# Performance work log

Hardware: AMD Instinct MI355X
Metric: run time of the kernel (lower is better)

## Reference

```python
import jax, jax.numpy as jnp
import numpy as np

N = 100000
E = 1600000
D_IN = 128
D_OUT = 128
EPS_GIN = 0.0  # GIN epsilon from __init__
LN_EPS = 1e-5
PROJ_EPS = 1e-9


def setup_inputs() -> dict:
    key = jax.random.key(0)
    ks = jax.random.split(key, 9)
    x = jax.random.normal(ks[0], (N, D_IN), dtype=jnp.float32)
    edge_index = jax.random.randint(ks[1], (2, E), 0, N, dtype=jnp.int64)
    edge_weight = jax.random.normal(ks[2], (E,), dtype=jnp.float32)
    # MLP params (Linear(in,out) -> ReLU -> Linear(out,out)), torch default-ish init
    s1 = 1.0 / np.sqrt(D_IN)
    s2 = 1.0 / np.sqrt(D_OUT)
    W1 = jax.random.uniform(ks[3], (D_IN, D_OUT), jnp.float32, -s1, s1)
    b1 = jax.random.uniform(ks[4], (D_OUT,), jnp.float32, -s1, s1)
    W2 = jax.random.uniform(ks[5], (D_OUT, D_OUT), jnp.float32, -s2, s2)
    b2 = jax.random.uniform(ks[6], (D_OUT,), jnp.float32, -s2, s2)
    gamma = jnp.ones((D_OUT,), jnp.float32)
    beta = jnp.zeros((D_OUT,), jnp.float32)
    return {"x": x, "edge_index": edge_index, "edge_weight": edge_weight,
            "W1": W1, "b1": b1, "W2": W2, "b2": b2, "gamma": gamma, "beta": beta}


def _aggregate(x, edge_index, edge_weight):
    # Per-target-node softmax over edge weights, then weighted projective average.
    src = edge_index[0]
    tgt = edge_index[1]
    n = x.shape[0]
    m = jax.ops.segment_max(edge_weight, tgt, num_segments=n)          # [N]
    ew = jnp.exp(edge_weight - m[tgt])                                  # [E], stable softmax numerator
    denom = jax.ops.segment_sum(ew, tgt, num_segments=n)               # [N]
    w = ew / denom[tgt]                                                 # [E], per-node softmax weights
    msg = w[:, None] * x[src]                                           # [E, D]
    agg = jax.ops.segment_sum(msg, tgt, num_segments=n)                # [N, D] weighted sum
    # projective_average: normalize the weighted combination to the unit sphere
    norm = jnp.linalg.norm(agg, axis=-1, keepdims=True)
    return agg / (norm + PROJ_EPS)                                      # zero rows stay zero


def _layer_norm(h, gamma, beta):
    mu = jnp.mean(h, axis=-1, keepdims=True)
    var = jnp.var(h, axis=-1, keepdims=True)
    return gamma * (h - mu) * jax.lax.rsqrt(var + LN_EPS) + beta


def reference(x, edge_index, edge_weight, W1, b1, W2, b2, gamma, beta):
    neigh = _aggregate(x, edge_index, edge_weight)
    combined = (1.0 + EPS_GIN) * x + neigh
    h = jnp.maximum(combined @ W1 + b1, 0.0)
    h = h @ W2 + b2
    h = _layer_norm(h, gamma, beta)
    # dropout: eval mode -> identity
    return h
```

## Files before the change

kernel.cpp:

```cpp
#include <hip/hip_runtime.h>
#include <hip/hip_bf16.h>

#define D 128
#define CH 2048
#define BSH 9
#define SLAB 9216
#define PREP_BLK 1024

typedef __attribute__((ext_vector_type(8))) short short8;
typedef __attribute__((ext_vector_type(4))) float f32x4;
typedef __attribute__((ext_vector_type(4))) int int4v;
typedef __attribute__((ext_vector_type(2))) int int2v;
typedef __attribute__((ext_vector_type(4))) float float4v;
typedef __attribute__((ext_vector_type(2))) float float2v;
typedef __attribute__((ext_vector_type(4))) unsigned uint4v;
typedef __attribute__((ext_vector_type(2))) unsigned uint2v;
typedef _Float16 half2_t __attribute__((ext_vector_type(2)));

__device__ __forceinline__ unsigned short us_bf16(float f) {
    return __bfloat16_as_ushort(__float2bfloat16(f));
}
__device__ __forceinline__ unsigned pack_bf16(float a, float b) {
    return (unsigned)us_bf16(a) | ((unsigned)us_bf16(b) << 16);
}
__device__ __forceinline__ unsigned pack_f16(float a, float b) {
    unsigned short ua = __builtin_bit_cast(unsigned short, (_Float16)a);
    unsigned short ub = __builtin_bit_cast(unsigned short, (_Float16)b);
    return (unsigned)ua | ((unsigned)ub << 16);
}
__device__ __forceinline__ float f16_lo(int y) {
    return (float)__builtin_bit_cast(_Float16, (unsigned short)(y & 0xffff));
}
__device__ __forceinline__ half2_t as_h2(unsigned u) {
    return __builtin_bit_cast(half2_t, u);
}
__device__ __forceinline__ int2v nt_load2(const int2* p) {
    return __builtin_nontemporal_load(reinterpret_cast<const int2v*>(p));
}

__global__ __launch_bounds__(256) void k_prepbinA(
    const int* __restrict__ src, const int* __restrict__ tgt,
    const float* __restrict__ ew, int* __restrict__ bcnt,
    int2* __restrict__ stage, int E, int nbuk, int nchunk,
    const float* __restrict__ x, unsigned* __restrict__ xh,
    unsigned* __restrict__ xq, int nf4,
    const float* __restrict__ W1, const float* __restrict__ W2,
    unsigned short* __restrict__ W1t, unsigned short* __restrict__ W2t)
{
    __shared__ int2 recs[CH];
    __shared__ unsigned short bslot[CH];
    __shared__ int sh[256];
    __shared__ int lbase[256];
    __shared__ int gofs[256];

    int tid = threadIdx.x;

    if (blockIdx.x >= (unsigned)nchunk) {
        int pb = blockIdx.x - nchunk;
        int i0 = pb * 256 + tid;
        int stride = PREP_BLK * 256;
        const float4v* x4 = reinterpret_cast<const float4v*>(x);
        uint2v* xh2 = reinterpret_cast<uint2v*>(xh);
        for (int i = i0; i < nf4; i += stride) {
            float4v v = x4[i];
            uint2v o;
            o.x = pack_f16(v.x, v.y);
            o.y = pack_f16(v.z, v.w);
            xh2[i] = o;
            int p = __builtin_amdgcn_cvt_pk_fp8_f32(v.x, v.y, 0, false);
            p = __builtin_amdgcn_cvt_pk_fp8_f32(v.z, v.w, p, true);
            xq[i] = (unsigned)p;
        }
        if (i0 < 16384) {
            int k = i0 >> 7, nn = i0 & 127;
            W1t[nn * 128 + k] = us_bf16(W1[i0]);
            W2t[nn * 128 + k] = us_bf16(W2[i0]);
        }
        return;
    }

    int c0 = blockIdx.x * CH;
    int chunkCnt = min(CH, E - c0);

    sh[tid] = 0;
    __syncthreads();

    int myb[8], mypos[8], mysrc[8]; unsigned myy[8];
    #pragma unroll
    for (int k = 0; k < 8; ++k) {
        int idx = k * 256 + tid;
        myb[k] = -1;
        if (idx < chunkCnt) {
            int e = c0 + idx;
            int t = __builtin_nontemporal_load(&tgt[e]);
            int b = t >> BSH;
            float expw = __expf(__builtin_nontemporal_load(&ew[e]));
            unsigned short h = __builtin_bit_cast(unsigned short, (_Float16)expw);
            myb[k] = b;
            myy[k] = ((unsigned)(t & ((1 << BSH) - 1)) << 16) | (unsigned)h;
            mysrc[k] = __builtin_nontemporal_load(&src[e]);
            mypos[k] = atomicAdd(&sh[b], 1);
        }
    }
    __syncthreads();
    int cnt_b = sh[tid];
    for (int off = 1; off < 256; off <<= 1) {
        int o = (tid >= off) ? sh[tid - off] : 0;
        __syncthreads();
        sh[tid] += o;
        __syncthreads();
    }
    int lb = sh[tid] - cnt_b;
    lbase[tid] = lb;
    if (cnt_b > 0 && tid < nbuk) {
        int gb = atomicAdd(&bcnt[tid], cnt_b) + tid * SLAB;
        gofs[tid] = gb - lb;
    }
    __syncthreads();
    #pragma unroll
    for (int k = 0; k < 8; ++k) {
        if (myb[k] >= 0) {
            int slot = lbase[myb[k]] + mypos[k];
            recs[slot] = make_int2(mysrc[k], (int)myy[k]);
            bslot[slot] = (unsigned short)myb[k];
        }
    }
    __syncthreads();
    for (int i = tid; i < chunkCnt; i += 256) {
        int b = bslot[i];
        stage[gofs[b] + i] = recs[i];
    }
}

__global__ __launch_bounds__(256) void k_binB(
    const int* __restrict__ bcnt, const int2* __restrict__ stage,
    int2* __restrict__ csr, int* __restrict__ rowptr, int n)
{
    __shared__ int lcnt[1 << BSH];
    __shared__ int sc[256];
    int b = blockIdx.x;
    int tid = threadIdx.x;
    int node0 = b << BSH;
    int nn = min(1 << BSH, n - node0);
    int s0 = b * SLAB;
    int s1 = s0 + bcnt[b];

    for (int j = tid; j < (1 << BSH); j += 256) lcnt[j] = 0;
    __syncthreads();

    for (int i = s0 + tid; i < s1; i += 256) {
        int2v rec = nt_load2(&stage[i]);
        atomicAdd(&lcnt[((unsigned)rec.y) >> 16], 1);
    }
    __syncthreads();

    int v0 = lcnt[2 * tid], v1 = lcnt[2 * tid + 1];
    int tsum = v0 + v1;
    sc[tid] = tsum;
    __syncthreads();
    for (int off = 1; off < 256; off <<= 1) {
        int o = (tid >= off) ? sc[tid - off] : 0;
        __syncthreads();
        sc[tid] += o;
        __syncthreads();
    }
    int excl = sc[tid] - tsum;
    int p0 = s0 + excl, p1 = s0 + excl + v0;
    if (2 * tid < nn)     rowptr[node0 + 2 * tid] = p0;
    if (2 * tid + 1 < nn) rowptr[node0 + 2 * tid + 1] = p1;
    __syncthreads();
    lcnt[2 * tid] = p0;
    lcnt[2 * tid + 1] = p1;
    __syncthreads();

    for (int i = s0 + tid; i < s1; i += 256) {
        int2v rec = nt_load2(&stage[i]);
        int pos = atomicAdd(&lcnt[((unsigned)rec.y) >> 16], 1);
        csr[pos] = make_int2(rec.x, rec.y);
    }
}

__global__ __launch_bounds__(256) void k_agg(
    const int* __restrict__ rowptr, const int* __restrict__ bcnt,
    const int2* __restrict__ csr,
    const uint4v* __restrict__ xq4, const uint4v* __restrict__ xh4,
    uint4v* __restrict__ cmb4, int n)
{
    int w = threadIdx.x >> 6;
    int lane = threadIdx.x & 63;
    int node = blockIdx.x * 4 + w;
    if (node >= n) node = n - 1;

    int b = node >> BSH;
    int r0 = rowptr[node];
    int r1;
    if ((((node + 1) & ((1 << BSH) - 1)) == 0) || (node + 1 >= n))
        r1 = b * SLAB + bcnt[b];
    else
        r1 = rowptr[node + 1];
    int cnt = r1 - r0;

    int eg = lane >> 3;
    int dg = lane & 7;

    float a[16];
    #pragma unroll
    for (int j = 0; j < 16; ++j) a[j] = 0.f;

    int last = (cnt > 0) ? cnt - 1 : 0;
    for (int base = 0; base < cnt; base += 32) {
        #pragma unroll
        for (int i = 0; i < 4; ++i) {
            if (base + i * 8 >= cnt) break;
            int e = base + i * 8 + eg;
            bool valid = e < cnt;
            int2v cr = nt_load2(&csr[r0 + (valid ? e : last)]);
            float wn = valid ? f16_lo(cr.y) : 0.f;
            uint4v q = xq4[cr.x * 8 + dg];
            #pragma unroll
            for (int h = 0; h < 4; ++h) {
                int word = (int)((h == 0) ? q.x : (h == 1) ? q.y : (h == 2) ? q.z : q.w);
                float2v flo = __builtin_amdgcn_cvt_pk_f32_fp8(word, false);
                float2v fhi = __builtin_amdgcn_cvt_pk_f32_fp8(word, true);
                a[h * 4 + 0] = fmaf(wn, flo.x, a[h * 4 + 0]);
                a[h * 4 + 1] = fmaf(wn, flo.y, a[h * 4 + 1]);
                a[h * 4 + 2] = fmaf(wn, fhi.x, a[h * 4 + 2]);
                a[h * 4 + 3] = fmaf(wn, fhi.y, a[h * 4 + 3]);
            }
        }
    }

    #pragma unroll
    for (int j = 0; j < 16; ++j) a[j] *= 0.00390625f;
    unsigned u[8];
    #pragma unroll
    for (int j = 0; j < 8; ++j)
        u[j] = __builtin_bit_cast(unsigned,
                   __builtin_amdgcn_cvt_pkrtz(a[2 * j], a[2 * j + 1]));
    #pragma unroll
    for (int m = 8; m <= 32; m <<= 1)
        #pragma unroll
        for (int j = 0; j < 8; ++j) {
            half2_t s = as_h2(u[j]) + as_h2((unsigned)__shfl_xor((int)u[j], m));
            u[j] = __builtin_bit_cast(unsigned, s);
        }
    float af[16];
    #pragma unroll
    for (int j = 0; j < 8; ++j) {
        half2_t s = as_h2(u[j]);
        af[2 * j] = (float)s.x;
        af[2 * j + 1] = (float)s.y;
    }

    float ss = 0.f;
    #pragma unroll
    for (int j = 0; j < 16; ++j) ss = fmaf(af[j], af[j], ss);
    #pragma unroll
    for (int m = 1; m <= 4; m <<= 1) ss += __shfl_xor(ss, m);
    float rn = 1.f / (sqrtf(ss) + 1e-9f);

    if (eg == 0) {
        #pragma unroll
        for (int h = 0; h < 2; ++h) {
            uint4v hx = xh4[node * 16 + dg * 2 + h];
            half2_t x0 = as_h2(hx.x), x1 = as_h2(hx.y), x2 = as_h2(hx.z), x3 = as_h2(hx.w);
            const float* ah = &af[h * 8];
            uint4v o;
            o.x = pack_bf16((float)x0.x + ah[0] * rn, (float)x0.y + ah[1] * rn);
            o.y = pack_bf16((float)x1.x + ah[2] * rn, (float)x1.y + ah[3] * rn);
            o.z = pack_bf16((float)x2.x + ah[4] * rn, (float)x2.y + ah[5] * rn);
            o.w = pack_bf16((float)x3.x + ah[6] * rn, (float)x3.y + ah[7] * rn);
            cmb4[node * 16 + dg * 2 + h] = o;
        }
    }
}

__global__ __launch_bounds__(256) void k_mlp(
    const uint4v* __restrict__ cmb4,
    const unsigned short* __restrict__ W1t, const unsigned short* __restrict__ W2t,
    const float* __restrict__ b1, const float* __restrict__ b2,
    const float* __restrict__ gamma, const float* __restrict__ beta,
    float* __restrict__ out, int n)
{
    __shared__ __align__(16) unsigned short sA[64][136];

    int node0 = blockIdx.x * 64;
    int w = threadIdx.x >> 6;
    int lane = threadIdx.x & 63;
    int lr = lane & 15;
    int lg = lane >> 4;
    int mr = w * 16;

    for (int idx = threadIdx.x; idx < 64 * 16; idx += 256) {
        int row = idx >> 4, seg = idx & 15;
        int gr = node0 + row; if (gr >= n) gr = n - 1;
        uint4v v = cmb4[gr * 16 + seg];
        *reinterpret_cast<uint4v*>(&sA[row][seg * 8]) = v;
    }
    __syncthreads();

    short8 aF[4];
    #pragma unroll
    for (int kt = 0; kt < 4; ++kt)
        aF[kt] = *reinterpret_cast<const short8*>(&sA[mr + lr][kt * 32 + lg * 8]);

    #pragma unroll
    for (int nt = 0; nt < 8; ++nt) {
        f32x4 c = {0.f, 0.f, 0.f, 0.f};
        #pragma unroll
        for (int kt = 0; kt < 4; ++kt) {
            short8 bF = *reinterpret_cast<const short8*>(
                &W1t[(nt * 16 + lr) * 128 + kt * 32 + lg * 8]);
            c = __builtin_amdgcn_mfma_f32_16x16x32_bf16(aF[kt], bF, c, 0, 0, 0);
        }
        float b1v = b1[nt * 16 + lr];
        #pragma unroll
        for (int reg = 0; reg < 4; ++reg) {
            float h = fmaxf(c[reg] + b1v, 0.f);
            sA[mr + lg * 4 + reg][nt * 16 + lr] = us_bf16(h);
        }
    }
    __syncthreads();

    short8 a2F[4];
    #pragma unroll
    for (int kt = 0; kt < 4; ++kt)
        a2F[kt] = *reinterpret_cast<const short8*>(&sA[mr + lr][kt * 32 + lg * 8]);

    f32x4 c2[8];
    float b2v[8], gv[8], bev[8];
    #pragma unroll
    for (int nt = 0; nt < 8; ++nt) {
        c2[nt] = (f32x4){0.f, 0.f, 0.f, 0.f};
        #pragma unroll
        for (int kt = 0; kt < 4; ++kt) {
            short8 bF = *reinterpret_cast<const short8*>(
                &W2t[(nt * 16 + lr) * 128 + kt * 32 + lg * 8]);
            c2[nt] = __builtin_amdgcn_mfma_f32_16x16x32_bf16(a2F[kt], bF, c2[nt], 0, 0, 0);
        }
        int col = nt * 16 + lr;
        b2v[nt] = b2[col]; gv[nt] = gamma[col]; bev[nt] = beta[col];
    }

    float rs[4] = {0.f, 0.f, 0.f, 0.f}, sq[4] = {0.f, 0.f, 0.f, 0.f};
    #pragma unroll
    for (int nt = 0; nt < 8; ++nt)
        #pragma unroll
        for (int reg = 0; reg < 4; ++reg) {
            float v = c2[nt][reg] + b2v[nt];
            rs[reg] += v; sq[reg] += v * v;
        }
    #pragma unroll
    for (int off = 1; off <= 8; off <<= 1)
        #pragma unroll
        for (int reg = 0; reg < 4; ++reg) {
            rs[reg] += __shfl_xor(rs[reg], off);
            sq[reg] += __shfl_xor(sq[reg], off);
        }
    float mu[4], rstd[4];
    #pragma unroll
    for (int reg = 0; reg < 4; ++reg) {
        mu[reg] = rs[reg] * (1.f / 128.f);
        float var = sq[reg] * (1.f / 128.f) - mu[reg] * mu[reg];
        rstd[reg] = rsqrtf(var + 1e-5f);
    }

    #pragma unroll
    for (int nt = 0; nt < 8; ++nt)
        #pragma unroll
        for (int reg = 0; reg < 4; ++reg) {
            int gr = node0 + mr + lg * 4 + reg;
            if (gr < n) {
                float v = c2[nt][reg] + b2v[nt];
                out[gr * 128 + nt * 16 + lr] = gv[nt] * (v - mu[reg]) * rstd[reg] + bev[nt];
            }
        }
}

extern "C" void kernel_launch(void* const* d_in, const int* in_sizes, int n_in,
                              void* d_out, int out_size, void* d_ws, size_t ws_size,
                              hipStream_t stream) {
    const float* x     = (const float*)d_in[0];
    const int*   ei    = (const int*)d_in[1];
    const float* ew    = (const float*)d_in[2];
    const float* W1    = (const float*)d_in[3];
    const float* b1    = (const float*)d_in[4];
    const float* W2    = (const float*)d_in[5];
    const float* b2    = (const float*)d_in[6];
    const float* gamma = (const float*)d_in[7];
    const float* beta  = (const float*)d_in[8];

    int n = in_sizes[0] / D;
    int E = in_sizes[2];
    const int* src = ei;
    const int* tgt = ei + E;

    int nbuk = (n + (1 << BSH) - 1) >> BSH;

    char* ws = (char*)d_ws;
    int2*     csr    = (int2*)ws;     ws += (size_t)nbuk * SLAB * sizeof(int2);
    unsigned* xh     = (unsigned*)ws; ws += (size_t)n * 64 * sizeof(unsigned);
    unsigned* xq     = (unsigned*)ws; ws += (size_t)n * 32 * sizeof(unsigned);
    unsigned* cmb    = (unsigned*)ws; ws += (size_t)n * 64 * sizeof(unsigned);
    unsigned short* W1t = (unsigned short*)ws; ws += 128 * 128 * sizeof(unsigned short);
    unsigned short* W2t = (unsigned short*)ws; ws += 128 * 128 * sizeof(unsigned short);
    int*      rowptr = (int*)ws;      ws += ((size_t)n + 1) * sizeof(int);
    int*      bcnt   = (int*)ws;      ws += 256 * sizeof(int);
    int2*     stage  = (int2*)cmb;

    hipMemsetAsync((void*)bcnt, 0, 256 * sizeof(int), stream);

    int nf4 = n * D / 4;
    int nchunk = (E + CH - 1) / CH;
    k_prepbinA<<<nchunk + PREP_BLK, 256, 0, stream>>>(
        src, tgt, ew, bcnt, stage, E, nbuk, nchunk,
        x, xh, xq, nf4, W1, W2, W1t, W2t);

    k_binB<<<nbuk, 256, 0, stream>>>(bcnt, stage, csr, rowptr, n);

    k_agg<<<(n + 3) / 4, 256, 0, stream>>>(rowptr, bcnt, csr,
                                           (const uint4v*)xq, (const uint4v*)xh,
                                           (uint4v*)cmb, n);

    k_mlp<<<(n + 63) / 64, 256, 0, stream>>>((const uint4v*)cmb, W1t, W2t,
                                             b1, b2, gamma, beta,
                                             (float*)d_out, n);
}
```

Before: 202.0 us.

## Fuse neighbor aggregation and MLP into one kernel via shared memory

Merges the aggregation and MLP kernels so each 512-thread block aggregates 64 nodes (8 per wave) directly into a shared-memory tile, then four waves run the MFMA MLP on it. This removes the global round trip of the bf16 combined buffer and one kernel launch. The staging buffer gets its own workspace region. The cost is that half the waves sit idle during the MLP phase, and each wave now processes nodes serially, with fewer blocks available to hide gather latency.

```diff
diff --git a/kernel.cpp b/kernel.cpp
--- a/kernel.cpp
+++ b/kernel.cpp
@@ -180,103 +180,10 @@
     }
 }
 
-__global__ __launch_bounds__(256) void k_agg(
+__global__ __launch_bounds__(512) void k_aggmlp(
     const int* __restrict__ rowptr, const int* __restrict__ bcnt,
     const int2* __restrict__ csr,
     const uint4v* __restrict__ xq4, const uint4v* __restrict__ xh4,
-    uint4v* __restrict__ cmb4, int n)
-{
-    int w = threadIdx.x >> 6;
-    int lane = threadIdx.x & 63;
-    int node = blockIdx.x * 4 + w;
-    if (node >= n) node = n - 1;
-
-    int b = node >> BSH;
-    int r0 = rowptr[node];
-    int r1;
-    if ((((node + 1) & ((1 << BSH) - 1)) == 0) || (node + 1 >= n))
-        r1 = b * SLAB + bcnt[b];
-    else
-        r1 = rowptr[node + 1];
-    int cnt = r1 - r0;
-
-    int eg = lane >> 3;
-    int dg = lane & 7;
-
-    float a[16];
-    #pragma unroll
-    for (int j = 0; j < 16; ++j) a[j] = 0.f;
-
-    int last = (cnt > 0) ? cnt - 1 : 0;
-    for (int base = 0; base < cnt; base += 32) {
-        #pragma unroll
-        for (int i = 0; i < 4; ++i) {
-            if (base + i * 8 >= cnt) break;
-            int e = base + i * 8 + eg;
-            bool valid = e < cnt;
-            int2v cr = nt_load2(&csr[r0 + (valid ? e : last)]);
-            float wn = valid ? f16_lo(cr.y) : 0.f;
-            uint4v q = xq4[cr.x * 8 + dg];
-            #pragma unroll
-            for (int h = 0; h < 4; ++h) {
-                int word = (int)((h == 0) ? q.x : (h == 1) ? q.y : (h == 2) ? q.z : q.w);
-                float2v flo = __builtin_amdgcn_cvt_pk_f32_fp8(word, false);
-                float2v fhi = __builtin_amdgcn_cvt_pk_f32_fp8(word, true);
-                a[h * 4 + 0] = fmaf(wn, flo.x, a[h * 4 + 0]);
-                a[h * 4 + 1] = fmaf(wn, flo.y, a[h * 4 + 1]);
-                a[h * 4 + 2] = fmaf(wn, fhi.x, a[h * 4 + 2]);
-                a[h * 4 + 3] = fmaf(wn, fhi.y, a[h * 4 + 3]);
-            }
-        }
-    }
-
-    #pragma unroll
-    for (int j = 0; j < 16; ++j) a[j] *= 0.00390625f;
-    unsigned u[8];
-    #pragma unroll
-    for (int j = 0; j < 8; ++j)
-        u[j] = __builtin_bit_cast(unsigned,
-                   __builtin_amdgcn_cvt_pkrtz(a[2 * j], a[2 * j + 1]));
-    #pragma unroll
-    for (int m = 8; m <= 32; m <<= 1)
-        #pragma unroll
-        for (int j = 0; j < 8; ++j) {
-            half2_t s = as_h2(u[j]) + as_h2((unsigned)__shfl_xor((int)u[j], m));
-            u[j] = __builtin_bit_cast(unsigned, s);
-        }
-    float af[16];
-    #pragma unroll
-    for (int j = 0; j < 8; ++j) {
-        half2_t s = as_h2(u[j]);
-        af[2 * j] = (float)s.x;
-        af[2 * j + 1] = (float)s.y;
-    }
-
-    float ss = 0.f;
-    #pragma unroll
-    for (int j = 0; j < 16; ++j) ss = fmaf(af[j], af[j], ss);
-    #pragma unroll
-    for (int m = 1; m <= 4; m <<= 1) ss += __shfl_xor(ss, m);
-    float rn = 1.f / (sqrtf(ss) + 1e-9f);
-
-    if (eg == 0) {
-        #pragma unroll
-        for (int h = 0; h < 2; ++h) {
-            uint4v hx = xh4[node * 16 + dg * 2 + h];
-            half2_t x0 = as_h2(hx.x), x1 = as_h2(hx.y), x2 = as_h2(hx.z), x3 = as_h2(hx.w);
-            const float* ah = &af[h * 8];
-            uint4v o;
-            o.x = pack_bf16((float)x0.x + ah[0] * rn, (float)x0.y + ah[1] * rn);
-            o.y = pack_bf16((float)x1.x + ah[2] * rn, (float)x1.y + ah[3] * rn);
-            o.z = pack_bf16((float)x2.x + ah[4] * rn, (float)x2.y + ah[5] * rn);
-            o.w = pack_bf16((float)x3.x + ah[6] * rn, (float)x3.y + ah[7] * rn);
-            cmb4[node * 16 + dg * 2 + h] = o;
-        }
-    }
-}
-
-__global__ __launch_bounds__(256) void k_mlp(
-    const uint4v* __restrict__ cmb4,
     const unsigned short* __restrict__ W1t, const unsigned short* __restrict__ W2t,
     const float* __restrict__ b1, const float* __restrict__ b2,
     const float* __restrict__ gamma, const float* __restrict__ beta,
@@ -284,20 +191,105 @@
 {
     __shared__ __align__(16) unsigned short sA[64][136];
 
+    int tid = threadIdx.x;
+    int wv = tid >> 6;
+    int lane = tid & 63;
     int node0 = blockIdx.x * 64;
-    int w = threadIdx.x >> 6;
-    int lane = threadIdx.x & 63;
+
+    int eg = lane >> 3;
+    int dg = lane & 7;
+
+    for (int r = wv * 8; r < wv * 8 + 8; ++r) {
+        int node = node0 + r;
+        if (node >= n) node = n - 1;
+
+        int b = node >> BSH;
+        int r0 = rowptr[node];
+        int r1;
+        if ((((node + 1) & ((1 << BSH) - 1)) == 0) || (node + 1 >= n))
+            r1 = b * SLAB + bcnt[b];
+        else
+            r1 = rowptr[node + 1];
+        int cnt = r1 - r0;
+
+        float a[16];
+        #pragma unroll
+        for (int j = 0; j < 16; ++j) a[j] = 0.f;
+
+        int last = (cnt > 0) ? cnt - 1 : 0;
+        for (int base = 0; base < cnt; base += 32) {
+            #pragma unroll
+            for (int i = 0; i < 4; ++i) {
+                if (base + i * 8 >= cnt) break;
+                int e = base + i * 8 + eg;
+                bool valid = e < cnt;
+                int2v cr = nt_load2(&csr[r0 + (valid ? e : last)]);
+                float wn = valid ? f16_lo(cr.y) : 0.f;
+                uint4v q = xq4[cr.x * 8 + dg];
+                #pragma unroll
+                for (int h = 0; h < 4; ++h) {
+                    int word = (int)((h == 0) ? q.x : (h == 1) ? q.y : (h == 2) ? q.z : q.w);
+                    float2v flo = __builtin_amdgcn_cvt_pk_f32_fp8(word, false);
+                    float2v fhi = __builtin_amdgcn_cvt_pk_f32_fp8(word, true);
+                    a[h * 4 + 0] = fmaf(wn, flo.x, a[h * 4 + 0]);
+                    a[h * 4 + 1] = fmaf(wn, flo.y, a[h * 4 + 1]);
+                    a[h * 4 + 2] = fmaf(wn, fhi.x, a[h * 4 + 2]);
+                    a[h * 4 + 3] = fmaf(wn, fhi.y, a[h * 4 + 3]);
+                }
+            }
+        }
+
+        #pragma unroll
+        for (int j = 0; j < 16; ++j) a[j] *= 0.00390625f;
+        unsigned u[8];
+        #pragma unroll
+        for (int j = 0; j < 8; ++j)
+            u[j] = __builtin_bit_cast(unsigned,
+                       __builtin_amdgcn_cvt_pkrtz(a[2 * j], a[2 * j + 1]));
+        #pragma unroll
+        for (int m = 8; m <= 32; m <<= 1)
+            #pragma unroll
+            for (int j = 0; j < 8; ++j) {
+                half2_t s = as_h2(u[j]) + as_h2((unsigned)__shfl_xor((int)u[j], m));
+                u[j] = __builtin_bit_cast(unsigned, s);
+            }
+        float af[16];
+        #pragma unroll
+        for (int j = 0; j < 8; ++j) {
+            half2_t s = as_h2(u[j]);
+            af[2 * j] = (float)s.x;
+            af[2 * j + 1] = (float)s.y;
+        }
+
+        float ss = 0.f;
+        #pragma unroll
+        for (int j = 0; j < 16; ++j) ss = fmaf(af[j], af[j], ss);
+        #pragma unroll
+        for (int m = 1; m <= 4; m <<= 1) ss += __shfl_xor(ss, m);
+        float rn = 1.f / (sqrtf(ss) + 1e-9f);
+
+        if (eg == 0) {
+            #pragma unroll
+            for (int h = 0; h < 2; ++h) {
+                uint4v hx = xh4[node * 16 + dg * 2 + h];
+                half2_t x0 = as_h2(hx.x), x1 = as_h2(hx.y), x2 = as_h2(hx.z), x3 = as_h2(hx.w);
+                const float* ah = &af[h * 8];
+                uint4v o;
+                o.x = pack_bf16((float)x0.x + ah[0] * rn, (float)x0.y + ah[1] * rn);
+                o.y = pack_bf16((float)x1.x + ah[2] * rn, (float)x1.y + ah[3] * rn);
+                o.z = pack_bf16((float)x2.x + ah[4] * rn, (float)x2.y + ah[5] * rn);
+                o.w = pack_bf16((float)x3.x + ah[6] * rn, (float)x3.y + ah[7] * rn);
+                *reinterpret_cast<uint4v*>(&sA[r][(dg * 2 + h) * 8]) = o;
+            }
+        }
+    }
+    __syncthreads();
+
+    if (wv >= 4) return;
+    int w = wv;
     int lr = lane & 15;
     int lg = lane >> 4;
     int mr = w * 16;
-
-    for (int idx = threadIdx.x; idx < 64 * 16; idx += 256) {
-        int row = idx >> 4, seg = idx & 15;
-        int gr = node0 + row; if (gr >= n) gr = n - 1;
-        uint4v v = cmb4[gr * 16 + seg];
-        *reinterpret_cast<uint4v*>(&sA[row][seg * 8]) = v;
-    }
-    __syncthreads();
 
     short8 aF[4];
     #pragma unroll
@@ -399,14 +391,13 @@
 
     char* ws = (char*)d_ws;
     int2*     csr    = (int2*)ws;     ws += (size_t)nbuk * SLAB * sizeof(int2);
+    int2*     stage  = (int2*)ws;     ws += (size_t)nbuk * SLAB * sizeof(int2);
     unsigned* xh     = (unsigned*)ws; ws += (size_t)n * 64 * sizeof(unsigned);
     unsigned* xq     = (unsigned*)ws; ws += (size_t)n * 32 * sizeof(unsigned);
-    unsigned* cmb    = (unsigned*)ws; ws += (size_t)n * 64 * sizeof(unsigned);
     unsigned short* W1t = (unsigned short*)ws; ws += 128 * 128 * sizeof(unsigned short);
     unsigned short* W2t = (unsigned short*)ws; ws += 128 * 128 * sizeof(unsigned short);
     int*      rowptr = (int*)ws;      ws += ((size_t)n + 1) * sizeof(int);
     int*      bcnt   = (int*)ws;      ws += 256 * sizeof(int);
-    int2*     stage  = (int2*)cmb;
 
     hipMemsetAsync((void*)bcnt, 0, 256 * sizeof(int), stream);
 
@@ -418,11 +409,7 @@
 
     k_binB<<<nbuk, 256, 0, stream>>>(bcnt, stage, csr, rowptr, n);
 
-    k_agg<<<(n + 3) / 4, 256, 0, stream>>>(rowptr, bcnt, csr,
-                                           (const uint4v*)xq, (const uint4v*)xh,
-                                           (uint4v*)cmb, n);
-
-    k_mlp<<<(n + 63) / 64, 256, 0, stream>>>((const uint4v*)cmb, W1t, W2t,
-                                             b1, b2, gamma, beta,
-                                             (float*)d_out, n);
-}
+    k_aggmlp<<<(n + 63) / 64, 512, 0, stream>>>(
+        rowptr, bcnt, csr, (const uint4v*)xq, (const uint4v*)xh,
+        W1t, W2t, b1, b2, gamma, beta, (float*)d_out, n);
+}
```

Measured after the change: 249.7 us. 1.24x slower.
